# Optimization experiments

Measured on AMD Instinct MI355X. Metric: run time of the kernel, lower is better.

## Reference

```python
import jax, jax.numpy as jnp
import numpy as np

EPS = 1e-7
TWO_PI = 2.0 * np.pi

K = 4096   # num gaussians
R = 8192   # num rays
MAP_SIZE = 100


def setup_inputs() -> dict:
    key = jax.random.key(0)
    k1, k2, k3, k4, k5, k6 = jax.random.split(key, 6)
    pos_raw = jax.random.normal(k1, (K, 2), dtype=jnp.float32)            # pre-sigmoid positions
    conc_raw = jax.random.normal(k2, (K,), dtype=jnp.float32)             # pre-softplus concentration
    scale_raw = 0.1 * jax.random.normal(k3, (K, 2), dtype=jnp.float32)    # log-scales
    rot_raw = jax.random.uniform(k4, (K,), dtype=jnp.float32) * TWO_PI    # rotation angles
    p_rays = jax.random.uniform(k5, (R, 2), dtype=jnp.float32) * MAP_SIZE # ray origins in map coords
    u = jax.random.normal(k6, (R, 2), dtype=jnp.float32)
    u_rays = u / jnp.linalg.norm(u, axis=-1, keepdims=True)               # unit ray directions
    return {"pos_raw": pos_raw, "conc_raw": conc_raw, "scale_raw": scale_raw,
            "rot_raw": rot_raw, "p_rays": p_rays, "u_rays": u_rays,
            "map_size": MAP_SIZE}


def _forward(pos_raw, conc_raw, scale_raw, rot_raw, p_rays, u_rays, map_size):
    # --- per-gaussian activations (GasSplattingModel getters) ---
    pos = jax.nn.sigmoid(pos_raw) * map_size           # (K,2)
    conc = jax.nn.softplus(conc_raw)                   # (K,)
    scale = jnp.exp(scale_raw)                         # (K,2)
    d0 = 1.0 / (scale[:, 0] ** 2 + EPS)                # diag of S^2 inverse
    d1 = 1.0 / (scale[:, 1] ** 2 + EPS)
    c, s = jnp.cos(rot_raw), jnp.sin(rot_raw)
    # Sigma^{-1} = R diag(d0,d1) R^T with R = [[c,-s],[s,c]]  (symmetric 2x2)
    m00 = c * c * d0 + s * s * d1                      # (K,)
    m01 = c * s * (d0 - d1)
    m11 = s * s * d0 + c * c * d1
    M = jnp.stack([m00, m01, m11], axis=0)             # (3,K) quadratic-form coeffs

    u0, u1 = u_rays[:, 0], u_rays[:, 1]
    p0, p1 = p_rays[:, 0], p_rays[:, 1]

    # quadratic-form features per ray, contracted with M via GEMM -> (R,K)
    qu = jnp.stack([u0 * u0, 2.0 * u0 * u1, u1 * u1], axis=1)        # (R,3)
    qp = jnp.stack([p0 * p0, 2.0 * p0 * p1, p1 * p1], axis=1)        # (R,3)
    qup = jnp.stack([u0 * p0, u0 * p1 + u1 * p0, u1 * p1], axis=1)   # (R,3)
    a = qu @ M          # u^T S u      (R,K)
    pSp = qp @ M        # p^T S p      (R,K)
    uSp = qup @ M       # u^T S p      (R,K)

    # S @ mu per gaussian -> (2,K)
    Sm = jnp.stack([m00 * pos[:, 0] + m01 * pos[:, 1],
                    m01 * pos[:, 0] + m11 * pos[:, 1]], axis=0)
    uSm = u_rays @ Sm   # u^T S mu     (R,K)
    pSm = p_rays @ Sm   # p^T S mu     (R,K)
    mSm = pos[:, 0] * Sm[0] + pos[:, 1] * Sm[1]        # mu^T S mu (K,)

    b = uSp - uSm                                      # u^T S (p - mu)
    c0 = pSp - 2.0 * pSm + mSm[None, :]                # (p-mu)^T S (p-mu)

    # closed-form line integral of conc * exp(-0.5 (x-mu)^T S (x-mu)) along ray
    dens = conc[None, :] * jnp.sqrt(TWO_PI / a) * jnp.exp(-0.5 * (c0 - b * b / a))
    return jnp.sum(dens, axis=-1)                      # (R,)


def reference(pos_raw, conc_raw, scale_raw, rot_raw, p_rays, u_rays, map_size):
    return _forward(pos_raw, conc_raw, scale_raw, rot_raw, p_rays, u_rays, map_size)
```

## Files before the change

### kernel.cpp

```cpp
#include <hip/hip_runtime.h>
#include <hip/hip_bf16.h>

#define EPS 1e-07f

#define BLOCK 256
#define IPT   4
#define SLICE 64

#define SQRT_HALF_LOG2E 0.84932180028801904f
#define LOG2_SQRT_2PI   1.32574806473616588f

typedef float v4f __attribute__((ext_vector_type(4)));

__global__ void precompute_gauss(const float* __restrict__ pos_raw,
                                 const float* __restrict__ conc_raw,
                                 const float* __restrict__ scale_raw,
                                 const float* __restrict__ rot_raw,
                                 const void*  __restrict__ map_size_p,
                                 float* __restrict__ gF,
                                 float* __restrict__ out,
                                 int K, int R)
{
    int k = blockIdx.x * blockDim.x + threadIdx.x;
    int nthreads = gridDim.x * blockDim.x;

    for (int i = k; i < R; i += nthreads) out[i] = 0.0f;

    if (k >= K) return;

    unsigned int msbits = *(const unsigned int*)map_size_p;
    float msf = __uint_as_float(msbits);
    float ms;
    if (msf >= 1e-3f && msf <= 1e9f) ms = msf;
    else                             ms = (float)(*(const int*)map_size_p);

    float pr0 = pos_raw[2*k],  pr1 = pos_raw[2*k+1];
    float pos0 = ms / (1.0f + expf(-pr0));
    float pos1 = ms / (1.0f + expf(-pr1));

    float cr = conc_raw[k];
    float conc = fmaxf(cr, 0.0f) + log1pf(expf(-fabsf(cr)));

    float s0 = expf(scale_raw[2*k]);
    float s1 = expf(scale_raw[2*k+1]);
    float d0 = 1.0f / (s0*s0 + EPS);
    float d1 = 1.0f / (s1*s1 + EPS);

    float rot = rot_raw[k];
    float c = cosf(rot), s = sinf(rot);

    float m00 = c*c*d0 + s*s*d1;
    float m01 = c*s*(d0 - d1);
    float m11 = s*s*d0 + c*c*d1;

    float det    = d0 * d1;
    float invdet = 1.0f / det;

    float cc = log2f(conc) + LOG2_SQRT_2PI - 0.5f * log2f(det);

    gF[0*K + k] = m00 * invdet;
    gF[1*K + k] = m01 * invdet;
    gF[2*K + k] = m11 * invdet;
    gF[3*K + k] = cc;
    gF[4*K + k] = pos0;
    gF[5*K + k] = pos1;
}

__global__ __launch_bounds__(BLOCK) void splat_main(
        const float* __restrict__ p_rays,
        const float* __restrict__ u_rays,
        const float* __restrict__ gF,
        float* __restrict__ out,
        int K)
{
    __shared__ float sF[6][SLICE];

    const int k0 = blockIdx.y * SLICE;
    const int nk = min(SLICE, K - k0);

    for (int i = threadIdx.x; i < 6*SLICE; i += BLOCK) {
        int f = i >> 6;
        int c = i & (SLICE - 1);
        if (c < nk) sF[f][c] = gF[f*K + k0 + c];
    }
    __syncthreads();

    const int rbase = blockIdx.x * (BLOCK * IPT) + threadIdx.x;

    float qu0[IPT], qu1[IPT], qu2[IPT], wt[IPT], su1[IPT], nsu0[IPT], acc[IPT];
    #pragma unroll
    for (int r = 0; r < IPT; ++r) {
        int ray = rbase + r * BLOCK;
        float2 p2 = *(const float2*)(p_rays + 2*ray);
        float2 u2 = *(const float2*)(u_rays + 2*ray);
        float p0 = p2.x, p1 = p2.y, u0 = u2.x, u1 = u2.y;
        qu0[r]  = u0*u0;
        qu1[r]  = 2.0f*u0*u1;
        qu2[r]  = u1*u1;
        wt[r]   =  SQRT_HALF_LOG2E * (u0*p1 - u1*p0);
        su1[r]  =  SQRT_HALF_LOG2E * u1;
        nsu0[r] = -SQRT_HALF_LOG2E * u0;
        acc[r]  = 0.0f;
    }

    const int nk4 = nk & ~3;
    for (int t4 = 0; t4 < nk4; t4 += 4) {
        v4f M00 = *(const v4f*)&sF[0][t4];
        v4f M01 = *(const v4f*)&sF[1][t4];
        v4f M11 = *(const v4f*)&sF[2][t4];
        v4f CC  = *(const v4f*)&sF[3][t4];
        v4f P0  = *(const v4f*)&sF[4][t4];
        v4f P1  = *(const v4f*)&sF[5][t4];

        #pragma unroll
        for (int g = 0; g < 4; ++g) {
            #pragma unroll
            for (int r = 0; r < IPT; ++r) {
                float a  = fmaf(qu2[r], M11[g], fmaf(qu1[r], M01[g], qu0[r] * M00[g]));
                float cr = fmaf(nsu0[r], P1[g], fmaf(su1[r], P0[g], wt[r]));
                float ra = __builtin_amdgcn_rsqf(a);
                float t  = cr * ra;
                float ar = fmaf(-t, t, CC[g]);
                float e  = __builtin_amdgcn_exp2f(ar);
                acc[r] = fmaf(ra, e, acc[r]);
            }
        }
    }
    for (int j = nk4; j < nk; ++j) {
        #pragma unroll
        for (int r = 0; r < IPT; ++r) {
            float a  = fmaf(qu2[r], sF[2][j], fmaf(qu1[r], sF[1][j], qu0[r] * sF[0][j]));
            float cr = fmaf(nsu0[r], sF[5][j], fmaf(su1[r], sF[4][j], wt[r]));
            float ra = __builtin_amdgcn_rsqf(a);
            float t  = cr * ra;
            float ar = fmaf(-t, t, sF[3][j]);
            float e  = __builtin_amdgcn_exp2f(ar);
            acc[r] = fmaf(ra, e, acc[r]);
        }
    }

    #pragma unroll
    for (int r = 0; r < IPT; ++r)
        atomicAdd(&out[rbase + r * BLOCK], acc[r]);
}

extern "C" void kernel_launch(void* const* d_in, const int* in_sizes, int n_in,
                              void* d_out, int out_size, void* d_ws, size_t ws_size,
                              hipStream_t stream)
{
    const float* pos_raw   = (const float*)d_in[0];
    const float* conc_raw  = (const float*)d_in[1];
    const float* scale_raw = (const float*)d_in[2];
    const float* rot_raw   = (const float*)d_in[3];
    const float* p_rays    = (const float*)d_in[4];
    const float* u_rays    = (const float*)d_in[5];
    const void*  map_size  = d_in[6];

    const int K = in_sizes[1];
    const int R = out_size;

    float* out = (float*)d_out;
    float* gF  = (float*)d_ws;

    {
        dim3 grid((K + BLOCK - 1) / BLOCK);
        precompute_gauss<<<grid, BLOCK, 0, stream>>>(pos_raw, conc_raw, scale_raw,
                                                     rot_raw, map_size,
                                                     gF, out, K, R);
    }
    {
        dim3 grid(R / (BLOCK * IPT), (K + SLICE - 1) / SLICE);
        splat_main<<<grid, BLOCK, 0, stream>>>(p_rays, u_rays, gF, out, K);
    }
}
```

Baseline: 23.02 us.

## Use fast intrinsics in precompute, interleave LDS layout, halve rays per thread

Several changes at once. The precompute kernel switches to fast-math intrinsics (__expf, __logf, __sinf, __cosf, __log2f) and runs with smaller 64-thread blocks so more blocks spread across CUs. The main kernel stores the shared gaussian features interleaved per group of four, fully unrolls the full-slice case, and processes two rays per thread instead of four, which doubles the grid. These aim to cut latency in the serial precompute and raise parallelism in the main loop, at the cost of some transcendental accuracy and less register reuse of each shared-memory load.

```diff
diff --git a/kernel.cpp b/kernel.cpp
--- a/kernel.cpp
+++ b/kernel.cpp
@@ -4,15 +4,17 @@
 #define EPS 1e-07f
 
 #define BLOCK 256
-#define IPT   4
+#define IPT   2
 #define SLICE 64
+#define PBLOCK 64
 
 #define SQRT_HALF_LOG2E 0.84932180028801904f
 #define LOG2_SQRT_2PI   1.32574806473616588f
 
 typedef float v4f __attribute__((ext_vector_type(4)));
 
-__global__ void precompute_gauss(const float* __restrict__ pos_raw,
+__global__ __launch_bounds__(PBLOCK) void precompute_gauss(
+                                 const float* __restrict__ pos_raw,
                                  const float* __restrict__ conc_raw,
                                  const float* __restrict__ scale_raw,
                                  const float* __restrict__ rot_raw,
@@ -35,19 +37,19 @@
     else                             ms = (float)(*(const int*)map_size_p);
 
     float pr0 = pos_raw[2*k],  pr1 = pos_raw[2*k+1];
-    float pos0 = ms / (1.0f + expf(-pr0));
-    float pos1 = ms / (1.0f + expf(-pr1));
+    float pos0 = ms / (1.0f + __expf(-pr0));
+    float pos1 = ms / (1.0f + __expf(-pr1));
 
     float cr = conc_raw[k];
-    float conc = fmaxf(cr, 0.0f) + log1pf(expf(-fabsf(cr)));
-
-    float s0 = expf(scale_raw[2*k]);
-    float s1 = expf(scale_raw[2*k+1]);
+    float conc = fmaxf(cr, 0.0f) + __logf(1.0f + __expf(-fabsf(cr)));
+
+    float s0 = __expf(scale_raw[2*k]);
+    float s1 = __expf(scale_raw[2*k+1]);
     float d0 = 1.0f / (s0*s0 + EPS);
     float d1 = 1.0f / (s1*s1 + EPS);
 
     float rot = rot_raw[k];
-    float c = cosf(rot), s = sinf(rot);
+    float c = __cosf(rot), s = __sinf(rot);
 
     float m00 = c*c*d0 + s*s*d1;
     float m01 = c*s*(d0 - d1);
@@ -56,7 +58,7 @@
     float det    = d0 * d1;
     float invdet = 1.0f / det;
 
-    float cc = log2f(conc) + LOG2_SQRT_2PI - 0.5f * log2f(det);
+    float cc = __log2f(conc) + LOG2_SQRT_2PI - 0.5f * __log2f(det);
 
     gF[0*K + k] = m00 * invdet;
     gF[1*K + k] = m01 * invdet;
@@ -73,7 +75,7 @@
         float* __restrict__ out,
         int K)
 {
-    __shared__ float sF[6][SLICE];
+    __shared__ float sG[SLICE/4][6][4];
 
     const int k0 = blockIdx.y * SLICE;
     const int nk = min(SLICE, K - k0);
@@ -81,7 +83,7 @@
     for (int i = threadIdx.x; i < 6*SLICE; i += BLOCK) {
         int f = i >> 6;
         int c = i & (SLICE - 1);
-        if (c < nk) sF[f][c] = gF[f*K + k0 + c];
+        if (c < nk) sG[c >> 2][f][c & 3] = gF[f*K + k0 + c];
     }
     __syncthreads();
 
@@ -103,41 +105,64 @@
         acc[r]  = 0.0f;
     }
 
-    const int nk4 = nk & ~3;
-    for (int t4 = 0; t4 < nk4; t4 += 4) {
-        v4f M00 = *(const v4f*)&sF[0][t4];
-        v4f M01 = *(const v4f*)&sF[1][t4];
-        v4f M11 = *(const v4f*)&sF[2][t4];
-        v4f CC  = *(const v4f*)&sF[3][t4];
-        v4f P0  = *(const v4f*)&sF[4][t4];
-        v4f P1  = *(const v4f*)&sF[5][t4];
-
+#define PAIR_BODY(M00, M01, M11, CC, P0, P1, g, r)                              \
+    {                                                                           \
+        float a_  = fmaf(qu2[r], (M11)[g], fmaf(qu1[r], (M01)[g],               \
+                                                qu0[r] * (M00)[g]));            \
+        float cr_ = fmaf(nsu0[r], (P1)[g], fmaf(su1[r], (P0)[g], wt[r]));       \
+        float ra_ = __builtin_amdgcn_rsqf(a_);                                  \
+        float t_  = cr_ * ra_;                                                  \
+        float ar_ = fmaf(-t_, t_, (CC)[g]);                                     \
+        float e_  = __builtin_amdgcn_exp2f(ar_);                                \
+        acc[r] = fmaf(ra_, e_, acc[r]);                                         \
+    }
+
+    if (nk == SLICE) {
         #pragma unroll
-        for (int g = 0; g < 4; ++g) {
+        for (int t4 = 0; t4 < SLICE/4; ++t4) {
+            v4f M00 = *(const v4f*)&sG[t4][0][0];
+            v4f M01 = *(const v4f*)&sG[t4][1][0];
+            v4f M11 = *(const v4f*)&sG[t4][2][0];
+            v4f CC  = *(const v4f*)&sG[t4][3][0];
+            v4f P0  = *(const v4f*)&sG[t4][4][0];
+            v4f P1  = *(const v4f*)&sG[t4][5][0];
+            #pragma unroll
+            for (int g = 0; g < 4; ++g)
+                #pragma unroll
+                for (int r = 0; r < IPT; ++r)
+                    PAIR_BODY(M00, M01, M11, CC, P0, P1, g, r)
+        }
+    } else {
+        const int ng = nk >> 2;
+        for (int t4 = 0; t4 < ng; ++t4) {
+            v4f M00 = *(const v4f*)&sG[t4][0][0];
+            v4f M01 = *(const v4f*)&sG[t4][1][0];
+            v4f M11 = *(const v4f*)&sG[t4][2][0];
+            v4f CC  = *(const v4f*)&sG[t4][3][0];
+            v4f P0  = *(const v4f*)&sG[t4][4][0];
+            v4f P1  = *(const v4f*)&sG[t4][5][0];
+            #pragma unroll
+            for (int g = 0; g < 4; ++g)
+                #pragma unroll
+                for (int r = 0; r < IPT; ++r)
+                    PAIR_BODY(M00, M01, M11, CC, P0, P1, g, r)
+        }
+        for (int j = ng << 2; j < nk; ++j) {
+            int t4 = j >> 2, g = j & 3;
             #pragma unroll
             for (int r = 0; r < IPT; ++r) {
-                float a  = fmaf(qu2[r], M11[g], fmaf(qu1[r], M01[g], qu0[r] * M00[g]));
-                float cr = fmaf(nsu0[r], P1[g], fmaf(su1[r], P0[g], wt[r]));
+                float a  = fmaf(qu2[r], sG[t4][2][g], fmaf(qu1[r], sG[t4][1][g],
+                                                           qu0[r] * sG[t4][0][g]));
+                float cr = fmaf(nsu0[r], sG[t4][5][g], fmaf(su1[r], sG[t4][4][g], wt[r]));
                 float ra = __builtin_amdgcn_rsqf(a);
                 float t  = cr * ra;
-                float ar = fmaf(-t, t, CC[g]);
+                float ar = fmaf(-t, t, sG[t4][3][g]);
                 float e  = __builtin_amdgcn_exp2f(ar);
                 acc[r] = fmaf(ra, e, acc[r]);
             }
         }
     }
-    for (int j = nk4; j < nk; ++j) {
-        #pragma unroll
-        for (int r = 0; r < IPT; ++r) {
-            float a  = fmaf(qu2[r], sF[2][j], fmaf(qu1[r], sF[1][j], qu0[r] * sF[0][j]));
-            float cr = fmaf(nsu0[r], sF[5][j], fmaf(su1[r], sF[4][j], wt[r]));
-            float ra = __builtin_amdgcn_rsqf(a);
-            float t  = cr * ra;
-            float ar = fmaf(-t, t, sF[3][j]);
-            float e  = __builtin_amdgcn_exp2f(ar);
-            acc[r] = fmaf(ra, e, acc[r]);
-        }
-    }
+#undef PAIR_BODY
 
     #pragma unroll
     for (int r = 0; r < IPT; ++r)
@@ -163,10 +188,10 @@
     float* gF  = (float*)d_ws;
 
     {
-        dim3 grid((K + BLOCK - 1) / BLOCK);
-        precompute_gauss<<<grid, BLOCK, 0, stream>>>(pos_raw, conc_raw, scale_raw,
-                                                     rot_raw, map_size,
-                                                     gF, out, K, R);
+        dim3 grid((K + PBLOCK - 1) / PBLOCK);
+        precompute_gauss<<<grid, PBLOCK, 0, stream>>>(pos_raw, conc_raw, scale_raw,
+                                                      rot_raw, map_size,
+                                                      gF, out, K, R);
     }
     {
         dim3 grid(R / (BLOCK * IPT), (K + SLICE - 1) / SLICE);
```

Result: faster. 22.23 us (-3.4%).
